# Optimization experiments

Hardware: AMD Instinct MI355X
Metric: run time of the kernel (lower is better)

Reference implementation:

```python
import jax, jax.numpy as jnp
import numpy as np

B, T, D = 4, 512, 192
CLAMP = 1e20


def setup_inputs() -> dict:
    key = jax.random.key(0)
    k1, k2 = jax.random.split(key, 2)
    x = jax.random.normal(k1, (B, T, D), dtype=jnp.float32)
    W = jax.random.normal(k2, (3 * D, D), dtype=jnp.float32) * 0.02  # c_attn weight
    b = jnp.zeros((3 * D,), dtype=jnp.float32)                       # c_attn bias
    S0 = jnp.zeros((B, 1, D, D), dtype=jnp.float32)                  # recurrent state S
    Z0 = jnp.zeros((B, 1, D), dtype=jnp.float32)                     # recurrent state Z
    return {"x": x, "W": W, "b": b, "S0": S0, "Z0": Z0}


def reference(x, W, b, S0, Z0):
    # c_attn: Linear(d_model -> 3*d_model), split into Q, K, V
    qkv = x @ W.T + b
    Q, K, V = jnp.split(qkv, 3, axis=2)
    # Phi: elu(x) + 1 feature map on Q and K
    Q = jax.nn.elu(Q) + 1.0
    K = jax.nn.elu(K) + 1.0

    # outer-product state: S[b,t] = clamp(cumsum_t K_t V_t^T) + S0
    outer = jnp.einsum('bti,btj->btij', K, V)                 # [B,T,D,D]
    S = jnp.clip(jnp.cumsum(outer, axis=1), -CLAMP, CLAMP) + S0
    Z = jnp.clip(jnp.cumsum(K, axis=1), -CLAMP, CLAMP) + Z0   # [B,T,D]

    numerator = jnp.einsum('bti,btil->btl', Q, S)             # [B,T,D]
    denominator = jnp.einsum('bti,bti->bt', Q, Z)[..., None] + 1e-5
    output = numerator / denominator

    Bz, Tz, F = K.shape
    S_last = S[:, -1].reshape(Bz, F * F)
    Z_last = Z[:, -1]
    return output, S_last, Z_last
```

## Files before the change

### kernel.cpp

```cpp
#include <hip/hip_runtime.h>
#include <cmath>

#define TB  512
#define DD  192
#define NCH 8
#define CKL 64

static __device__ __forceinline__ float elu1(float v) {
    return v > 0.0f ? v + 1.0f : expf(v);
}

__global__ __launch_bounds__(256) void k_qkv(
    const float* __restrict__ x, const float* __restrict__ W,
    const float* __restrict__ bias,
    float* __restrict__ Qp, float* __restrict__ Kp, float* __restrict__ Vp)
{
    __shared__ float xs[32][68];
    __shared__ float wsT[64 * 64];
    const int tid = threadIdx.x;
    const int n0 = blockIdx.x * 32;
    const int m0 = blockIdx.y * 64;
    const int a  = tid >> 4;
    const int c  = tid & 15;

    float acc[2][4];
    #pragma unroll
    for (int r = 0; r < 2; ++r)
        #pragma unroll
        for (int s = 0; s < 4; ++s) acc[r][s] = 0.f;

    for (int kb = 0; kb < DD; kb += 64) {
        #pragma unroll
        for (int p = 0; p < 2; ++p) {
            int q = p * 256 + tid;
            int row = q >> 4, c4 = (q & 15) * 4;
            *(float4*)&xs[row][c4] = *(const float4*)&x[(n0 + row) * DD + kb + c4];
        }
        #pragma unroll
        for (int p = 0; p < 4; ++p) {
            int q = p * 256 + tid;
            int mrow = q >> 4, kidx = q & 15;
            float4 wv = *(const float4*)&W[(m0 + mrow) * DD + kb + kidx * 4];
            int g = (mrow >> 2) ^ kidx;
            int pcol = g * 4 + (mrow & 3);
            wsT[(kidx * 4 + 0) * 64 + pcol] = wv.x;
            wsT[(kidx * 4 + 1) * 64 + pcol] = wv.y;
            wsT[(kidx * 4 + 2) * 64 + pcol] = wv.z;
            wsT[(kidx * 4 + 3) * 64 + pcol] = wv.w;
        }
        __syncthreads();
        #pragma unroll
        for (int kk = 0; kk < 64; kk += 4) {
            float4 xv0 = *(const float4*)&xs[a][kk];
            float4 xv1 = *(const float4*)&xs[16 + a][kk];
            const int g = (c ^ ((kk >> 2) & 15)) * 4;
            float x0[4] = {xv0.x, xv0.y, xv0.z, xv0.w};
            float x1[4] = {xv1.x, xv1.y, xv1.z, xv1.w};
            #pragma unroll
            for (int j = 0; j < 4; ++j) {
                float4 wk = *(const float4*)&wsT[(kk + j) * 64 + g];
                acc[0][0] += x0[j] * wk.x; acc[0][1] += x0[j] * wk.y;
                acc[0][2] += x0[j] * wk.z; acc[0][3] += x0[j] * wk.w;
                acc[1][0] += x1[j] * wk.x; acc[1][1] += x1[j] * wk.y;
                acc[1][2] += x1[j] * wk.z; acc[1][3] += x1[j] * wk.w;
            }
        }
        __syncthreads();
    }

    const int reg  = m0 / DD;
    float* dst = (reg == 0) ? Qp : (reg == 1 ? Kp : Vp);
    const int mloc = (m0 % DD) + c * 4;
    #pragma unroll
    for (int r = 0; r < 2; ++r) {
        int n = n0 + r * 16 + a;
        float v0 = acc[r][0] + bias[m0 + c * 4 + 0];
        float v1 = acc[r][1] + bias[m0 + c * 4 + 1];
        float v2 = acc[r][2] + bias[m0 + c * 4 + 2];
        float v3 = acc[r][3] + bias[m0 + c * 4 + 3];
        if (reg < 2) { v0 = elu1(v0); v1 = elu1(v1); v2 = elu1(v2); v3 = elu1(v3); }
        *(float4*)&dst[n * DD + mloc] = make_float4(v0, v1, v2, v3);
    }
}

__global__ __launch_bounds__(256) void k_mid(
    const float* __restrict__ Kp, const float* __restrict__ Vp,
    const float* __restrict__ Qp,
    float* __restrict__ Mws, float* __restrict__ zws,
    float* __restrict__ Aws, float* __restrict__ denws)
{
    __shared__ float sm[64 * 196];
    const int tid  = threadIdx.x;
    const int bc   = blockIdx.x;
    const int role = blockIdx.y;
    const int base = bc * CKL;

    if (role < 6) {
        const int ih = role / 3, jh = role % 3;
        float (*Ks)[100] = (float (*)[100])sm;
        float (*Vs)[68]  = (float (*)[68])(sm + 6400);

        #pragma unroll
        for (int p = 0; p < 6; ++p) {
            int q = p * 256 + tid;
            int row = q / 24, c4 = (q % 24) * 4;
            *(float4*)&Ks[row][c4] = *(const float4*)&Kp[(base + row) * DD + ih * 96 + c4];
        }
        #pragma unroll
        for (int p = 0; p < 4; ++p) {
            int q = p * 256 + tid;
            int row = q >> 4, c4 = (q & 15) * 4;
            *(float4*)&Vs[row][c4] = *(const float4*)&Vp[(base + row) * DD + jh * 64 + c4];
        }
        __syncthreads();

        const int ig = tid >> 4, jg = tid & 15;
        const int iL = ig * 6;
        float acc[6][4];
        #pragma unroll
        for (int i = 0; i < 6; ++i)
            #pragma unroll
            for (int j = 0; j < 4; ++j) acc[i][j] = 0.f;

        #pragma unroll 4
        for (int t = 0; t < CKL; ++t) {
            float4 v = *(const float4*)&Vs[t][jg * 4];
            float2 k0 = *(const float2*)&Ks[t][iL + 0];
            float2 k1 = *(const float2*)&Ks[t][iL + 2];
            float2 k2 = *(const float2*)&Ks[t][iL + 4];
            float kv[6] = {k0.x, k0.y, k1.x, k1.y, k2.x, k2.y};
            #pragma unroll
            for (int i = 0; i < 6; ++i) {
                acc[i][0] += kv[i] * v.x;
                acc[i][1] += kv[i] * v.y;
                acc[i][2] += kv[i] * v.z;
                acc[i][3] += kv[i] * v.w;
            }
        }

        float* Mout = Mws + (size_t)bc * DD * DD;
        const int j0 = jh * 64 + jg * 4;
        #pragma unroll
        for (int i = 0; i < 6; ++i)
            *(float4*)&Mout[(ih * 96 + iL + i) * DD + j0] =
                make_float4(acc[i][0], acc[i][1], acc[i][2], acc[i][3]);

        if (jh == 0 && tid < 96) {
            float s = 0.f;
            #pragma unroll 8
            for (int t = 0; t < CKL; ++t) s += Ks[t][tid];
            zws[bc * DD + ih * 96 + tid] = s;
        }
    } else {
        const int tq = role - 6;
        const int tbase = tq * 16;
        float (*Ks)[196] = (float (*)[196])sm;

        #pragma unroll
        for (int p = 0; p < 12; ++p) {
            int q = p * 256 + tid;
            int row = q / 48, c4 = (q % 48) * 4;
            *(float4*)&Ks[row][c4] = *(const float4*)&Kp[(base + row) * DD + c4];
        }
        __syncthreads();

        const int trow = tid >> 4, tc = tid & 15;
        const int tg = tbase + trow;
        const float* Qrow = Qp + (size_t)(base + tg) * DD;
        float acc[4];
        #pragma unroll
        for (int s = 0; s < 4; ++s) acc[s] = 0.f;

        #pragma unroll 4
        for (int k = 0; k < DD; k += 4) {
            float4 qv = *(const float4*)&Qrow[k];
            #pragma unroll
            for (int s = 0; s < 4; ++s) {
                float4 kv = *(const float4*)&Ks[tc * 4 + s][k];
                acc[s] += qv.x*kv.x + qv.y*kv.y + qv.z*kv.z + qv.w*kv.w;
            }
        }

        float av[4], psum = 0.f;
        #pragma unroll
        for (int s = 0; s < 4; ++s) {
            int tau = tc * 4 + s;
            av[s] = (tau <= tg) ? acc[s] : 0.f;
            psum += av[s];
        }
        *(float4*)&Aws[bc * 4096 + tg * 64 + tc * 4] =
            make_float4(av[0], av[1], av[2], av[3]);
        #pragma unroll
        for (int off = 1; off < 16; off <<= 1)
            psum += __shfl_xor(psum, off, 16);
        if (tc == 0) denws[base + tg] = psum;
    }
}

__global__ __launch_bounds__(256) void k_prefix(
    const float* __restrict__ Mws, const float* __restrict__ S0,
    const float* __restrict__ zws, const float* __restrict__ Z0,
    float* __restrict__ Sb, float* __restrict__ Zb,
    float* __restrict__ Slast, float* __restrict__ Zlast)
{
    const int w = blockIdx.x;
    const int b = w / 144;
    const int e = (w % 144) * 256 + threadIdx.x;
    float acc = S0[b * DD * DD + e];
    #pragma unroll
    for (int cc = 0; cc < NCH; ++cc) {
        Sb[(size_t)(b * NCH + cc) * DD * DD + e] = acc;
        acc += Mws[(size_t)(b * NCH + cc) * DD * DD + e];
    }
    Slast[b * DD * DD + e] = acc;

    if ((w % 144) == 0 && threadIdx.x < DD) {
        const int i = threadIdx.x;
        float za = Z0[b * DD + i];
        #pragma unroll
        for (int cc = 0; cc < NCH; ++cc) {
            Zb[(b * NCH + cc) * DD + i] = za;
            za += zws[(b * NCH + cc) * DD + i];
        }
        Zlast[b * DD + i] = za;
    }
}

__global__ __launch_bounds__(256) void k_output(
    const float* __restrict__ Qp, const float* __restrict__ Vp,
    const float* __restrict__ Aws, const float* __restrict__ denws,
    const float* __restrict__ Sb, const float* __restrict__ Zb,
    float* __restrict__ out)
{
    __shared__ float Ss[DD][64];
    __shared__ float As[16][64];
    __shared__ float Zs[DD];
    const int tid   = threadIdx.x;
    const int bc    = blockIdx.x;
    const int tq    = blockIdx.y;
    const int lq    = blockIdx.z;
    const int base  = bc * CKL;
    const int tbase = tq * 16;

    const float* Sbc = Sb + (size_t)bc * DD * DD + lq * 64;
    #pragma unroll
    for (int p = 0; p < 12; ++p) {
        int q = p * 256 + tid;
        int row = q >> 4, c4 = (q & 15) * 4;
        *(float4*)&Ss[row][c4] = *(const float4*)&Sbc[row * DD + c4];
    }
    {
        int row = tid >> 4, c4 = (tid & 15) * 4;
        *(float4*)&As[row][c4] =
            *(const float4*)&Aws[bc * 4096 + (tbase + row) * 64 + c4];
    }
    if (tid < 48)
        *(float4*)&Zs[tid * 4] = *(const float4*)&Zb[bc * DD + tid * 4];
    __syncthreads();

    const int tg = tid >> 4, lg = tid & 15;
    const int trow = tbase + tg;
    const int l0 = lq * 64 + lg * 4;
    float ax = 0.f, ay = 0.f, az = 0.f, aw = 0.f, dacc = 0.f;

    const float* Vb = Vp + (size_t)base * DD;
    #pragma unroll 8
    for (int tau = 0; tau < CKL; ++tau) {
        float a = As[tg][tau];
        float4 v = *(const float4*)&Vb[tau * DD + l0];
        ax += a * v.x; ay += a * v.y; az += a * v.z; aw += a * v.w;
    }

    const float* Qrow = Qp + (size_t)(base + trow) * DD;
    #pragma unroll 4
    for (int i = 0; i < DD; i += 4) {
        float4 qv = *(const float4*)&Qrow[i];
        float4 zv = *(const float4*)&Zs[i];
        dacc += qv.x*zv.x + qv.y*zv.y + qv.z*zv.z + qv.w*zv.w;
        float qq[4] = {qv.x, qv.y, qv.z, qv.w};
        #pragma unroll
        for (int u = 0; u < 4; ++u) {
            float4 s = *(const float4*)&Ss[i + u][lg * 4];
            ax += qq[u] * s.x; ay += qq[u] * s.y;
            az += qq[u] * s.z; aw += qq[u] * s.w;
        }
    }

    float den = denws[base + trow] + dacc + 1e-5f;
    float inv = 1.f / den;
    *(float4*)&out[(size_t)(base + trow) * DD + l0] =
        make_float4(ax * inv, ay * inv, az * inv, aw * inv);
}

extern "C" void kernel_launch(void* const* d_in, const int* in_sizes, int n_in,
                              void* d_out, int out_size, void* d_ws, size_t ws_size,
                              hipStream_t stream)
{
    const float* x  = (const float*)d_in[0];
    const float* W  = (const float*)d_in[1];
    const float* bb = (const float*)d_in[2];
    const float* S0 = (const float*)d_in[3];
    const float* Z0 = (const float*)d_in[4];

    float* out   = (float*)d_out;
    float* Slast = out + (size_t)4 * TB * DD;
    float* Zlast = Slast + (size_t)4 * DD * DD;

    float* ws   = (float*)d_ws;
    float* Qp   = ws;
    float* Kp   = Qp + (size_t)4 * TB * DD;
    float* Vp   = Kp + (size_t)4 * TB * DD;
    float* Mws  = Vp + (size_t)4 * TB * DD;
    float* Sbse = Mws + (size_t)4 * NCH * DD * DD;
    float* zws  = Sbse + (size_t)4 * NCH * DD * DD;
    float* Zbse = zws + (size_t)4 * NCH * DD;
    float* Aws  = Zbse + (size_t)4 * NCH * DD;
    float* denw = Aws + (size_t)4 * NCH * CKL * CKL;

    k_qkv   <<<dim3(64, 9),    256, 0, stream>>>(x, W, bb, Qp, Kp, Vp);
    k_mid   <<<dim3(32, 10),   256, 0, stream>>>(Kp, Vp, Qp, Mws, zws, Aws, denw);
    k_prefix<<<dim3(576),      256, 0, stream>>>(Mws, S0, zws, Z0, Sbse, Zbse, Slast, Zlast);
    k_output<<<dim3(32, 4, 3), 256, 0, stream>>>(Qp, Vp, Aws, denw, Sbse, Zbse, out);
}
```

Measured before the change: 99.74 us.

## Fuse chunk-state prefix sum into output kernel and stage Q in LDS

Removes the separate prefix kernel and the materialized per-chunk state buffers. Each output block now rebuilds its S column slice by summing S0 and the earlier chunk M matrices directly, writing Slast and Zlast from the last chunk. The output grid is re-tiled to 16 columns by 64 rows per block, with A and V staged in shared memory. The mid kernel's attention-score role also stages Q rows in LDS. The cost is redundant reads of M across chunks, up to 7 per block, traded for one fewer launch and less global traffic.

```diff
diff --git a/kernel.cpp b/kernel.cpp
--- a/kernel.cpp
+++ b/kernel.cpp
@@ -89,7 +89,7 @@
     float* __restrict__ Mws, float* __restrict__ zws,
     float* __restrict__ Aws, float* __restrict__ denws)
 {
-    __shared__ float sm[64 * 196];
+    __shared__ float sm[64 * 196 + 16 * 196];
     const int tid  = threadIdx.x;
     const int bc   = blockIdx.x;
     const int role = blockIdx.y;
@@ -155,6 +155,7 @@
         const int tq = role - 6;
         const int tbase = tq * 16;
         float (*Ks)[196] = (float (*)[196])sm;
+        float (*Qs)[196] = (float (*)[196])(sm + 64 * 196);
 
         #pragma unroll
         for (int p = 0; p < 12; ++p) {
@@ -162,18 +163,23 @@
             int row = q / 48, c4 = (q % 48) * 4;
             *(float4*)&Ks[row][c4] = *(const float4*)&Kp[(base + row) * DD + c4];
         }
+        #pragma unroll
+        for (int p = 0; p < 3; ++p) {
+            int q = p * 256 + tid;
+            int row = q / 48, c4 = (q % 48) * 4;
+            *(float4*)&Qs[row][c4] = *(const float4*)&Qp[(base + tbase + row) * DD + c4];
+        }
         __syncthreads();
 
         const int trow = tid >> 4, tc = tid & 15;
         const int tg = tbase + trow;
-        const float* Qrow = Qp + (size_t)(base + tg) * DD;
         float acc[4];
         #pragma unroll
         for (int s = 0; s < 4; ++s) acc[s] = 0.f;
 
         #pragma unroll 4
         for (int k = 0; k < DD; k += 4) {
-            float4 qv = *(const float4*)&Qrow[k];
+            float4 qv = *(const float4*)&Qs[trow][k];
             #pragma unroll
             for (int s = 0; s < 4; ++s) {
                 float4 kv = *(const float4*)&Ks[tc * 4 + s][k];
@@ -197,98 +203,108 @@
     }
 }
 
-__global__ __launch_bounds__(256) void k_prefix(
-    const float* __restrict__ Mws, const float* __restrict__ S0,
-    const float* __restrict__ zws, const float* __restrict__ Z0,
-    float* __restrict__ Sb, float* __restrict__ Zb,
-    float* __restrict__ Slast, float* __restrict__ Zlast)
-{
-    const int w = blockIdx.x;
-    const int b = w / 144;
-    const int e = (w % 144) * 256 + threadIdx.x;
-    float acc = S0[b * DD * DD + e];
-    #pragma unroll
-    for (int cc = 0; cc < NCH; ++cc) {
-        Sb[(size_t)(b * NCH + cc) * DD * DD + e] = acc;
-        acc += Mws[(size_t)(b * NCH + cc) * DD * DD + e];
-    }
-    Slast[b * DD * DD + e] = acc;
-
-    if ((w % 144) == 0 && threadIdx.x < DD) {
-        const int i = threadIdx.x;
-        float za = Z0[b * DD + i];
-        #pragma unroll
-        for (int cc = 0; cc < NCH; ++cc) {
-            Zb[(b * NCH + cc) * DD + i] = za;
-            za += zws[(b * NCH + cc) * DD + i];
-        }
-        Zlast[b * DD + i] = za;
-    }
-}
-
-__global__ __launch_bounds__(256) void k_output(
+__global__ __launch_bounds__(256) void k_out(
     const float* __restrict__ Qp, const float* __restrict__ Vp,
     const float* __restrict__ Aws, const float* __restrict__ denws,
-    const float* __restrict__ Sb, const float* __restrict__ Zb,
-    float* __restrict__ out)
+    const float* __restrict__ Mws, const float* __restrict__ zws,
+    const float* __restrict__ S0, const float* __restrict__ Z0,
+    float* __restrict__ out, float* __restrict__ Slast, float* __restrict__ Zlast)
 {
-    __shared__ float Ss[DD][64];
-    __shared__ float As[16][64];
+    __shared__ float As[64][68];
+    __shared__ float Ss[DD][16];
+    __shared__ float Vs[CKL][16];
     __shared__ float Zs[DD];
-    const int tid   = threadIdx.x;
-    const int bc    = blockIdx.x;
-    const int tq    = blockIdx.y;
-    const int lq    = blockIdx.z;
-    const int base  = bc * CKL;
-    const int tbase = tq * 16;
-
-    const float* Sbc = Sb + (size_t)bc * DD * DD + lq * 64;
+    const int tid = threadIdx.x;
+    const int bc  = blockIdx.x;
+    const int lq  = blockIdx.y;
+    const int b   = bc >> 3, c = bc & 7;
+    const int base = bc * CKL;
+    const int lofs = lq * 16;
+
     #pragma unroll
-    for (int p = 0; p < 12; ++p) {
+    for (int p = 0; p < 4; ++p) {
         int q = p * 256 + tid;
         int row = q >> 4, c4 = (q & 15) * 4;
-        *(float4*)&Ss[row][c4] = *(const float4*)&Sbc[row * DD + c4];
+        *(float4*)&As[row][c4] = *(const float4*)&Aws[bc * 4096 + row * 64 + c4];
     }
     {
-        int row = tid >> 4, c4 = (tid & 15) * 4;
-        *(float4*)&As[row][c4] =
-            *(const float4*)&Aws[bc * 4096 + (tbase + row) * 64 + c4];
-    }
-    if (tid < 48)
-        *(float4*)&Zs[tid * 4] = *(const float4*)&Zb[bc * DD + tid * 4];
+        int row = tid >> 2, c4 = (tid & 3) * 4;
+        *(float4*)&Vs[row][c4] = *(const float4*)&Vp[(base + row) * DD + lofs + c4];
+    }
+    {
+        float4 r[3];
+        #pragma unroll
+        for (int p = 0; p < 3; ++p) {
+            int q = p * 256 + tid;
+            int row = q >> 2, c4 = (q & 3) * 4;
+            r[p] = *(const float4*)&S0[(size_t)b * DD * DD + row * DD + lofs + c4];
+        }
+        for (int cc = 0; cc < c; ++cc) {
+            const float* Mc = Mws + (size_t)(b * NCH + cc) * DD * DD;
+            #pragma unroll
+            for (int p = 0; p < 3; ++p) {
+                int q = p * 256 + tid;
+                int row = q >> 2, c4 = (q & 3) * 4;
+                float4 m = *(const float4*)&Mc[row * DD + lofs + c4];
+                r[p].x += m.x; r[p].y += m.y; r[p].z += m.z; r[p].w += m.w;
+            }
+        }
+        #pragma unroll
+        for (int p = 0; p < 3; ++p) {
+            int q = p * 256 + tid;
+            int row = q >> 2, c4 = (q & 3) * 4;
+            *(float4*)&Ss[row][c4] = r[p];
+        }
+        if (c == NCH - 1) {
+            const float* M7 = Mws + (size_t)(b * NCH + 7) * DD * DD;
+            #pragma unroll
+            for (int p = 0; p < 3; ++p) {
+                int q = p * 256 + tid;
+                int row = q >> 2, c4 = (q & 3) * 4;
+                float4 m = *(const float4*)&M7[row * DD + lofs + c4];
+                *(float4*)&Slast[(size_t)b * DD * DD + row * DD + lofs + c4] =
+                    make_float4(r[p].x + m.x, r[p].y + m.y, r[p].z + m.z, r[p].w + m.w);
+            }
+        }
+    }
+    if (tid < DD) {
+        float z = Z0[b * DD + tid];
+        for (int cc = 0; cc < c; ++cc)
+            z += zws[(b * NCH + cc) * DD + tid];
+        Zs[tid] = z;
+        if (c == NCH - 1 && lq == 0)
+            Zlast[b * DD + tid] = z + zws[(b * NCH + 7) * DD + tid];
+    }
     __syncthreads();
 
-    const int tg = tid >> 4, lg = tid & 15;
-    const int trow = tbase + tg;
-    const int l0 = lq * 64 + lg * 4;
+    const int t  = tid >> 2;
+    const int lg = (tid & 3) * 4;
     float ax = 0.f, ay = 0.f, az = 0.f, aw = 0.f, dacc = 0.f;
 
-    const float* Vb = Vp + (size_t)base * DD;
-    #pragma unroll 8
+    #pragma unroll 16
     for (int tau = 0; tau < CKL; ++tau) {
-        float a = As[tg][tau];
-        float4 v = *(const float4*)&Vb[tau * DD + l0];
+        float a = As[t][tau];
+        float4 v = *(const float4*)&Vs[tau][lg];
         ax += a * v.x; ay += a * v.y; az += a * v.z; aw += a * v.w;
     }
 
-    const float* Qrow = Qp + (size_t)(base + trow) * DD;
+    const float* Qrow = Qp + (size_t)(base + t) * DD;
     #pragma unroll 4
     for (int i = 0; i < DD; i += 4) {
         float4 qv = *(const float4*)&Qrow[i];
-        float4 zv = *(const float4*)&Zs[i];
-        dacc += qv.x*zv.x + qv.y*zv.y + qv.z*zv.z + qv.w*zv.w;
         float qq[4] = {qv.x, qv.y, qv.z, qv.w};
         #pragma unroll
         for (int u = 0; u < 4; ++u) {
-            float4 s = *(const float4*)&Ss[i + u][lg * 4];
+            float4 s = *(const float4*)&Ss[i + u][lg];
             ax += qq[u] * s.x; ay += qq[u] * s.y;
             az += qq[u] * s.z; aw += qq[u] * s.w;
-        }
-    }
-
-    float den = denws[base + trow] + dacc + 1e-5f;
+            dacc += qq[u] * Zs[i + u];
+        }
+    }
+
+    float den = denws[base + t] + dacc + 1e-5f;
     float inv = 1.f / den;
-    *(float4*)&out[(size_t)(base + trow) * DD + l0] =
+    *(float4*)&out[(size_t)(base + t) * DD + lofs + lg] =
         make_float4(ax * inv, ay * inv, az * inv, aw * inv);
 }
 
@@ -311,14 +327,12 @@
     float* Kp   = Qp + (size_t)4 * TB * DD;
     float* Vp   = Kp + (size_t)4 * TB * DD;
     float* Mws  = Vp + (size_t)4 * TB * DD;
-    float* Sbse = Mws + (size_t)4 * NCH * DD * DD;
-    float* zws  = Sbse + (size_t)4 * NCH * DD * DD;
-    float* Zbse = zws + (size_t)4 * NCH * DD;
-    float* Aws  = Zbse + (size_t)4 * NCH * DD;
+    float* zws  = Mws + (size_t)4 * NCH * DD * DD;
+    float* Aws  = zws + (size_t)4 * NCH * DD;
     float* denw = Aws + (size_t)4 * NCH * CKL * CKL;
 
-    k_qkv   <<<dim3(64, 9),    256, 0, stream>>>(x, W, bb, Qp, Kp, Vp);
-    k_mid   <<<dim3(32, 10),   256, 0, stream>>>(Kp, Vp, Qp, Mws, zws, Aws, denw);
-    k_prefix<<<dim3(576),      256, 0, stream>>>(Mws, S0, zws, Z0, Sbse, Zbse, Slast, Zlast);
-    k_output<<<dim3(32, 4, 3), 256, 0, stream>>>(Qp, Vp, Aws, denw, Sbse, Zbse, out);
-}
+    k_qkv<<<dim3(64, 9),  256, 0, stream>>>(x, W, bb, Qp, Kp, Vp);
+    k_mid<<<dim3(32, 10), 256, 0, stream>>>(Kp, Vp, Qp, Mws, zws, Aws, denw);
+    k_out<<<dim3(32, 12), 256, 0, stream>>>(Qp, Vp, Aws, denw, Mws, zws,
+                                            S0, Z0, out, Slast, Zlast);
+}
```

Result: slower. 102.2 us (+2.4%).
